# Performance work log

Hardware: AMD Instinct MI355X
Metric: run time of the kernel (lower is better)

The kernel has to match this reference:

```python
import jax, jax.numpy as jnp
import numpy as np

B, T, D, H, L = 8, 64, 128, 4, 4
G = B * T            # 512 frame-graphs
NPG = 200            # nodes per graph
N = G * NPG          # 102400 nodes
E = 8 * N            # 819200 edges
FIN, HID = 2, 64
DH = D // H
NCLS = 2


def setup_inputs():
    key = jax.random.key(0)
    ks = jax.random.split(key, 16)
    w = lambda k, s: (jax.random.normal(k, s) * 0.05).astype(jnp.float32)
    x = jax.random.normal(ks[0], (N, FIN), dtype=jnp.float32)
    g = jax.random.randint(ks[1], (E,), 0, G)
    src = (g * NPG + jax.random.randint(ks[2], (E,), 0, NPG)).astype(jnp.int32)
    dst = (g * NPG + jax.random.randint(ks[3], (E,), 0, NPG)).astype(jnp.int32)
    node_graph = (jnp.arange(N) // NPG).astype(jnp.int32)
    return dict(
        x=x, edge_src=src, edge_dst=dst, node_graph=node_graph,
        gW1=w(ks[4], (FIN, HID)), gb1=jnp.zeros((HID,), jnp.float32),
        ln1g=jnp.ones((HID,), jnp.float32), ln1b=jnp.zeros((HID,), jnp.float32),
        gW2=w(ks[5], (HID, HID)), gb2=jnp.zeros((HID,), jnp.float32),
        ln2g=jnp.ones((HID,), jnp.float32), ln2b=jnp.zeros((HID,), jnp.float32),
        gW3=w(ks[6], (HID, D)), gb3=jnp.zeros((D,), jnp.float32),
        tWqkv=w(ks[7], (L, 3 * D, D)), tbqkv=jnp.zeros((L, 3 * D), jnp.float32),
        tWo=w(ks[8], (L, D, D)), tbo=jnp.zeros((L, D), jnp.float32),
        tg1=jnp.ones((L, D), jnp.float32), tb1=jnp.zeros((L, D), jnp.float32),
        tg2=jnp.ones((L, D), jnp.float32), tb2=jnp.zeros((L, D), jnp.float32),
        tWf1=w(ks[9], (L, 4 * D, D)), tbf1=jnp.zeros((L, 4 * D), jnp.float32),
        tWf2=w(ks[10], (L, D, 4 * D)), tbf2=jnp.zeros((L, D), jnp.float32),
        hW1=w(ks[11], (D // 2, D)), hb1=jnp.zeros((D // 2,), jnp.float32),
        hW2=w(ks[12], (NCLS, D // 2)), hb2=jnp.zeros((NCLS,), jnp.float32),
    )


def _ln(x, g, b, eps=1e-5):
    m = jnp.mean(x, -1, keepdims=True)
    v = jnp.var(x, -1, keepdims=True)
    return (x - m) * jax.lax.rsqrt(v + eps) * g + b


def _forward(x, edge_src, edge_dst, node_graph, gW1, gb1, ln1g, ln1b, gW2, gb2,
             ln2g, ln2b, gW3, gb3, tWqkv, tbqkv, tWo, tbo, tg1, tb1, tg2, tb2,
             tWf1, tbf1, tWf2, tbf2, hW1, hb1, hW2, hb2):
    # --- GCN encoder (PyG GCNConv: sym-normalized A with self loops) ---
    loops = jnp.arange(N, dtype=jnp.int32)
    src = jnp.concatenate([edge_src, loops])
    dst = jnp.concatenate([edge_dst, loops])
    deg = jnp.zeros((N,), x.dtype).at[dst].add(1.0)
    dinv = jax.lax.rsqrt(deg)
    norm = (dinv[src] * dinv[dst])[:, None]

    def gcn(h, W, b):
        h = h @ W  # transform first (smaller message dim when FIN < HID)
        return jax.ops.segment_sum(h[src] * norm, dst, num_segments=N) + b

    h = _ln(jax.nn.relu(gcn(x, gW1, gb1)), ln1g, ln1b)
    h = _ln(jax.nn.relu(gcn(h, gW2, gb2)), ln2g, ln2b)
    h = gcn(h, gW3, gb3)  # (N, D)

    # per-graph mean readout (replaces the python loop in the original)
    cnt = jax.ops.segment_sum(jnp.ones((N,), h.dtype), node_graph, num_segments=G)
    emb = jax.ops.segment_sum(h, node_graph, num_segments=G) / cnt[:, None]
    seq = emb.reshape(B, T, D)

    # --- sinusoidal positional encoding ---
    pos = jnp.arange(T, dtype=jnp.float32)[:, None]
    div = jnp.exp(jnp.arange(0, D, 2, dtype=jnp.float32) * (-np.log(10000.0) / D))
    pe = jnp.zeros((T, D), jnp.float32)
    pe = pe.at[:, 0::2].set(jnp.sin(pos * div)).at[:, 1::2].set(jnp.cos(pos * div))
    seq = seq + pe

    # --- TransformerEncoder (post-norm, relu FFN, batch_first) ---
    scale = 1.0 / np.sqrt(DH)
    for l in range(L):
        qkv = seq @ tWqkv[l].T + tbqkv[l]
        q, k, v = jnp.split(qkv, 3, axis=-1)
        q = q.reshape(B, T, H, DH).transpose(0, 2, 1, 3)
        k = k.reshape(B, T, H, DH).transpose(0, 2, 1, 3)
        v = v.reshape(B, T, H, DH).transpose(0, 2, 1, 3)
        att = jax.nn.softmax(jnp.einsum('bhqd,bhkd->bhqk', q, k) * scale, axis=-1)
        a = jnp.einsum('bhqk,bhkd->bhqd', att, v).transpose(0, 2, 1, 3).reshape(B, T, D)
        seq = _ln(seq + a @ tWo[l].T + tbo[l], tg1[l], tb1[l])
        f = jax.nn.relu(seq @ tWf1[l].T + tbf1[l]) @ tWf2[l].T + tbf2[l]
        seq = _ln(seq + f, tg2[l], tb2[l])

    pooled = jnp.mean(seq, axis=1)  # mask=None path -> plain temporal mean
    return jax.nn.relu(pooled @ hW1.T + hb1) @ hW2.T + hb2  # (B, NCLS)


def reference(x, edge_src, edge_dst, node_graph, gW1, gb1, ln1g, ln1b, gW2, gb2,
              ln2g, ln2b, gW3, gb3, tWqkv, tbqkv, tWo, tbo, tg1, tb1, tg2, tb2,
              tWf1, tbf1, tWf2, tbf2, hW1, hb1, hW2, hb2):
    return _forward(x, edge_src, edge_dst, node_graph, gW1, gb1, ln1g, ln1b,
                    gW2, gb2, ln2g, ln2b, gW3, gb3, tWqkv, tbqkv, tWo, tbo,
                    tg1, tb1, tg2, tb2, tWf1, tbf1, tWf2, tbf2, hW1, hb1, hW2, hb2)
```

## Files before the change

### kernel.cpp

```cpp
#include <hip/hip_runtime.h>

#define NN   102400
#define EE   819200
#define GG   512
#define NPG  200
#define DD   128
#define TT   64
#define BB   8
#define LL   4
#define NB_A   320
#define ECH_A  2560
#define SCAP 2560
#define NSLOT 16
#define CHK  50

typedef unsigned int uint;

static __device__ __forceinline__ void wave_sum64_2(float& a, float& b) {
#pragma unroll
    for (int off = 32; off > 0; off >>= 1) {
        a += __shfl_xor(a, off, 64);
        b += __shfl_xor(b, off, 64);
    }
}


__global__ __launch_bounds__(256) void k_a1(const int* __restrict__ src,
                                            int* __restrict__ hist) {
    __shared__ int h[GG];
    int tid = threadIdx.x;
    h[tid] = 0; h[tid + 256] = 0;
    __syncthreads();
    int base = blockIdx.x * ECH_A;
#pragma unroll
    for (int it = 0; it < ECH_A / 256; ++it)
        atomicAdd(&h[src[base + it * 256 + tid] / NPG], 1);
    __syncthreads();
    hist[blockIdx.x * GG + tid] = h[tid];
    hist[blockIdx.x * GG + tid + 256] = h[tid + 256];
}

__global__ __launch_bounds__(64) void k_a2a(const int* __restrict__ hist,
                                            int* __restrict__ gcnt) {
    int g = blockIdx.x, lane = threadIdx.x;
    int s = 0;
#pragma unroll
    for (int i = 0; i < NB_A / 64; ++i) s += hist[(i * 64 + lane) * GG + g];
#pragma unroll
    for (int off = 32; off > 0; off >>= 1) s += __shfl_xor(s, off, 64);
    if (lane == 0) gcnt[g] = s;
}

__global__ __launch_bounds__(512) void k_a2b(const int* __restrict__ gcnt,
                                             int* __restrict__ goff) {
    __shared__ int sm[GG];
    int g = threadIdx.x;
    int c = gcnt[g];
    sm[g] = c;
    __syncthreads();
    for (int d = 1; d < GG; d <<= 1) {
        int v = (g >= d) ? sm[g - d] : 0;
        __syncthreads();
        sm[g] += v;
        __syncthreads();
    }
    goff[g] = sm[g] - c;
    if (g == GG - 1) goff[GG] = sm[g];
}

__global__ __launch_bounds__(512) void k_a2c(const int* __restrict__ hist,
                                             const int* __restrict__ goff,
                                             int* __restrict__ off2) {
    int g = blockIdx.x * 8 + (threadIdx.x >> 6);
    int lane = threadIdx.x & 63;
    int running = goff[g];
#pragma unroll
    for (int cchunk = 0; cchunk < NB_A / 64; ++cchunk) {
        int b = cchunk * 64 + lane;
        int v = hist[b * GG + g];
        int s = v;
#pragma unroll
        for (int off = 1; off < 64; off <<= 1) {
            int t_ = __shfl_up(s, off, 64);
            if (lane >= off) s += t_;
        }
        off2[b * GG + g] = running + s - v;
        running += __shfl(s, 63, 64);
    }
}

__global__ __launch_bounds__(256) void k_a3(const int* __restrict__ src,
                                            const int* __restrict__ dst,
                                            const int* __restrict__ off2,
                                            uint* __restrict__ gpack) {
    __shared__ int cur[GG];
    int tid = threadIdx.x;
    cur[tid] = off2[blockIdx.x * GG + tid];
    cur[tid + 256] = off2[blockIdx.x * GG + tid + 256];
    __syncthreads();
    int base = blockIdx.x * ECH_A;
#pragma unroll
    for (int it = 0; it < ECH_A / 256; ++it) {
        int e = base + it * 256 + tid;
        int s = src[e], d = dst[e];
        int g = s / NPG;
        int pos = atomicAdd(&cur[g], 1);
        gpack[pos] = ((uint)(s - g * NPG) << 8) | (uint)(d - g * NPG);
    }
}

__global__ __launch_bounds__(256) void k_bsort(
    const float* __restrict__ x, const int* __restrict__ goff,
    const uint* __restrict__ gpack, const float* __restrict__ W1,
    const float* __restrict__ gb1, const float* __restrict__ lng,
    const float* __restrict__ lnb, uint2* __restrict__ slots,
    uint2* __restrict__ ovf, int* __restrict__ ovfcnt,
    float* __restrict__ wgtv, float* __restrict__ hout) {
    int g = ((blockIdx.x & 7) << 6) | (blockIdx.x >> 3);
    __shared__ float2 xs[NPG];
    __shared__ float2 aggl[NPG];
    __shared__ int cnt2[NPG];
    __shared__ int lnoff[NPG + 1];
    __shared__ int cur[NPG];
    __shared__ float rsq[NPG];
    __shared__ float cwl[NPG];
    __shared__ uint srec[SCAP];
    __shared__ int sm[256];
    __shared__ uint2 ovfl[128];
    __shared__ int ovfcur;
    int tid = threadIdx.x;
    int base = goff[g], E = goff[g + 1] - base;
    const float2* x2 = (const float2*)x;
    if (tid < NPG) { xs[tid] = x2[g * NPG + tid]; cnt2[tid] = 0; cwl[tid] = 0.f; }
    if (tid == 0) ovfcur = 0;
    __syncthreads();
    for (int i = tid; i < E; i += 256) atomicAdd(&cnt2[gpack[base + i] & 255u], 1);
    __syncthreads();
    int c = (tid < NPG) ? cnt2[tid] : 0;
    sm[tid] = c;
    __syncthreads();
    for (int d = 1; d < 256; d <<= 1) {
        int v = (tid >= d) ? sm[tid - d] : 0;
        __syncthreads();
        sm[tid] += v;
        __syncthreads();
    }
    if (tid < NPG) {
        lnoff[tid] = sm[tid] - c;
        cur[tid] = sm[tid] - c;
        rsq[tid] = rsqrtf((float)(c + 1));
    }
    if (tid == 0) lnoff[NPG] = E;
    __syncthreads();
    for (int i = tid; i < E; i += 256) {
        uint r = gpack[base + i];
        int pos = atomicAdd(&cur[r & 255u], 1);
        srec[pos] = r;
    }
    __syncthreads();
    for (int i = tid; i < E; i += 256) {
        uint r = srec[i];
        atomicAdd(&cwl[r >> 8], rsq[r >> 8] * rsq[r & 255u]);
    }
    __syncthreads();
    {
        uint2* sbase = &slots[(size_t)g * NPG * NSLOT];
        for (int li = tid; li < NPG * NSLOT; li += 256) {
            int n = li >> 4, s = li & 15;
            int e0 = lnoff[n];
            int En = lnoff[n + 1] - e0;
            float rd = rsq[n];
            uint2 v;
            if (s == 0) {
                v = make_uint2((uint)(g * NPG + n), __float_as_uint(rd * rd));
            } else if (s - 1 < En) {
                uint r = srec[e0 + s - 1];
                int ls = (int)(r >> 8);
                v = make_uint2((uint)(g * NPG + ls), __float_as_uint(rsq[ls] * rd));
            } else {
                v = make_uint2((uint)(g * NPG + n), 0u);
            }
            sbase[li] = v;
        }
    }
    if (tid < NPG) {
        float rd = rsq[tid];
        float dv = rd * rd;
        float ax = xs[tid].x * dv, ay = xs[tid].y * dv;
        int e0 = lnoff[tid], e1 = lnoff[tid + 1];
        for (int e = e0; e < e1; ++e) {
            uint r = srec[e];
            int ls = (int)(r >> 8);
            float w = rsq[ls] * rd;
            ax += xs[ls].x * w;
            ay += xs[ls].y * w;
        }
        for (int e = e0 + NSLOT - 1; e < e1; ++e) {
            uint r = srec[e];
            int ls = (int)(r >> 8);
            int p = atomicAdd(&ovfcur, 1);
            if (p < 128)
                ovfl[p] = make_uint2(((uint)tid << 17) | (uint)(g * NPG + ls),
                                     __float_as_uint(rsq[ls] * rd));
        }
        aggl[tid] = make_float2(ax, ay);
        wgtv[g * NPG + tid] = cwl[tid] + dv;
    }
    __syncthreads();
    int nov = ovfcur < 128 ? ovfcur : 128;
    if (tid == 0) ovfcnt[g] = nov;
    if (tid < nov) ovf[g * 128 + tid] = ovfl[tid];
    int lane = tid & 63, wid = tid >> 6;
    float w0 = W1[lane], w1 = W1[64 + lane];
    float gbj = gb1[lane], lgj = lng[lane], lbj = lnb[lane];
    for (int i = wid; i < NPG; i += 4) {
        float2 a = aggl[i];
        float u = fmaxf(a.x * w0 + a.y * w1 + gbj, 0.f);
        float s2 = u, q2 = u * u;
        wave_sum64_2(s2, q2);
        float mean = s2 * (1.f / 64.f);
        float var = q2 * (1.f / 64.f) - mean * mean;
        hout[(size_t)(g * NPG + i) * 64 + lane] = (u - mean) * rsqrtf(var + 1e-5f) * lgj + lbj;
    }
}


__global__ __launch_bounds__(256) void k_agg_lin_pool(
    const float* __restrict__ t, const float* __restrict__ W,
    const float* __restrict__ gb, const float* __restrict__ lng,
    const float* __restrict__ lnb, const uint2* __restrict__ slots,
    const uint2* __restrict__ ovf, const int* __restrict__ ovfcnt,
    const float* __restrict__ wgtv, float* __restrict__ pooled) {
    int c = ((blockIdx.x & 7) << 8) | (blockIdx.x >> 3);
    int n0 = c * CHK;
    int g = c >> 2, lbase = (c & 3) * CHK;
    __shared__ float hs[CHK][64];
    __shared__ uint2 slt[CHK][NSLOT];
    __shared__ float wgt[CHK];
    __shared__ float red[4][64];
    int tid = threadIdx.x, lane = tid & 63, wid = tid >> 6;
    int grp = lane >> 4, fq = lane & 15;
    float wreg[64];
#pragma unroll
    for (int k = 0; k < 64; ++k) wreg[k] = W[k * 64 + lane];
    {
        const float4* s4 = (const float4*)&slots[(size_t)n0 * NSLOT];
        float4* d4 = (float4*)slt;
        for (int i = tid; i < CHK * NSLOT / 2; i += 256) d4[i] = s4[i];
    }
    if (tid < CHK) wgt[tid] = wgtv[n0 + tid];
    __syncthreads();
#pragma unroll 2
    for (int i = wid; i < CHK; i += 4) {
        float4 acc = make_float4(0.f, 0.f, 0.f, 0.f);
#pragma unroll
        for (int r = 0; r < 4; ++r) {
            uint2 s = slt[i][r * 4 + grp];
            float w = __uint_as_float(s.y);
            float4 tv = *(const float4*)&t[(size_t)s.x * 64 + fq * 4];
            acc.x += tv.x * w; acc.y += tv.y * w;
            acc.z += tv.z * w; acc.w += tv.w * w;
        }
        acc.x += __shfl_xor(acc.x, 16); acc.y += __shfl_xor(acc.y, 16);
        acc.z += __shfl_xor(acc.z, 16); acc.w += __shfl_xor(acc.w, 16);
        acc.x += __shfl_xor(acc.x, 32); acc.y += __shfl_xor(acc.y, 32);
        acc.z += __shfl_xor(acc.z, 32); acc.w += __shfl_xor(acc.w, 32);
        if (grp == 0) *(float4*)&hs[i][fq * 4] = acc;
    }
    __syncthreads();
    int nov = ovfcnt[g];
    if (nov && wid == 0) {
        for (int k = 0; k < nov; ++k) {
            uint2 r = ovf[g * 128 + k];
            int ld = r.x >> 17;
            if (ld >= lbase && ld < lbase + CHK)
                hs[ld - lbase][lane] +=
                    t[(size_t)(r.x & 0x1FFFFu) * 64 + lane] * __uint_as_float(r.y);
        }
    }
    __syncthreads();
    float gbj = gb[lane], lgj = lng[lane], lbj = lnb[lane];
    float psum = 0.f;
    for (int i = wid; i < CHK; i += 4) {
        const float4* hrow = (const float4*)&hs[i][0];
        float a0 = 0.f, a1 = 0.f;
#pragma unroll
        for (int k4 = 0; k4 < 16; k4 += 2) {
            float4 h0 = hrow[k4], h1 = hrow[k4 + 1];
            a0 += h0.x * wreg[4 * k4] + h0.y * wreg[4 * k4 + 1] +
                  h0.z * wreg[4 * k4 + 2] + h0.w * wreg[4 * k4 + 3];
            a1 += h1.x * wreg[4 * k4 + 4] + h1.y * wreg[4 * k4 + 5] +
                  h1.z * wreg[4 * k4 + 6] + h1.w * wreg[4 * k4 + 7];
        }
        float u = fmaxf(a0 + a1 + gbj, 0.f);
        float s = u, q = u * u;
        wave_sum64_2(s, q);
        float mean = s * (1.f / 64.f);
        float var = q * (1.f / 64.f) - mean * mean;
        float h = (u - mean) * rsqrtf(var + 1e-5f) * lgj + lbj;
        psum += h * wgt[i];
    }
    red[wid][lane] = psum;
    __syncthreads();
    if (tid < 64)
        atomicAdd(&pooled[g * 64 + tid],
                  red[0][tid] + red[1][tid] + red[2][tid] + red[3][tid]);
}

__global__ __launch_bounds__(128) void k_emb(
    const float* __restrict__ pooled, const float* __restrict__ W3,
    const float* __restrict__ b3, float* __restrict__ seq) {
    int g = blockIdx.x, d = threadIdx.x;
    __shared__ float ps[64];
    if (d < 64) ps[d] = pooled[g * 64 + d] * (1.f / NPG);
    __syncthreads();
    float a = b3[d];
#pragma unroll 8
    for (int k = 0; k < 64; ++k) a += ps[k] * W3[k * DD + d];
    float freq = expf((float)(d & ~1) * (-9.210340371976184f / 128.f));
    float ang = (float)(g & (TT - 1)) * freq;
    a += (d & 1) ? cosf(ang) : sinf(ang);
    seq[(size_t)g * DD + d] = a;
}


__global__ __launch_bounds__(128) void k_qkv(
    const float* __restrict__ seq, const float* __restrict__ Wqkv,
    const float* __restrict__ bqkv, float* __restrict__ qkvb) {
    int m = blockIdx.x, tid = threadIdx.x;
    __shared__ float row[128];
    row[tid] = seq[(size_t)m * DD + tid];
    __syncthreads();
    const float4* r4 = (const float4*)row;
    float acc0 = bqkv[tid], acc1 = bqkv[tid + 128], acc2 = bqkv[tid + 256];
    const float4* w0 = (const float4*)&Wqkv[(size_t)tid * DD];
    const float4* w1 = (const float4*)&Wqkv[(size_t)(tid + 128) * DD];
    const float4* w2 = (const float4*)&Wqkv[(size_t)(tid + 256) * DD];
#pragma unroll
    for (int k = 0; k < 32; ++k) {
        float4 a = r4[k];
        float4 x0 = w0[k], x1 = w1[k], x2 = w2[k];
        acc0 += a.x * x0.x + a.y * x0.y + a.z * x0.z + a.w * x0.w;
        acc1 += a.x * x1.x + a.y * x1.y + a.z * x1.z + a.w * x1.w;
        acc2 += a.x * x2.x + a.y * x2.y + a.z * x2.z + a.w * x2.w;
    }
    float* ob = qkvb + (size_t)m * 384;
    ob[tid] = acc0;
    ob[tid + 128] = acc1;
    ob[tid + 256] = acc2;
}

__global__ __launch_bounds__(256) void k_attn(const float* __restrict__ qkvb,
                                              float* __restrict__ abuf) {
    int bh = blockIdx.x >> 2, quad = blockIdx.x & 3;
    int b = bh >> 2, h = bh & 3;
    __shared__ float Ks[64][36], Vs[64][36];
    __shared__ float Ss[16][68];
    int tid = threadIdx.x;
    const float* base = qkvb + (size_t)(b * 64) * 384 + h * 32;
    for (int li = tid; li < 512; li += 256) {
        int r = li >> 3, cc = li & 7;
        *(float4*)&Ks[r][cc * 4] = *(const float4*)&base[(size_t)r * 384 + 128 + cc * 4];
        *(float4*)&Vs[r][cc * 4] = *(const float4*)&base[(size_t)r * 384 + 256 + cc * 4];
    }
    __syncthreads();
    int ql = tid >> 4, kl = tid & 15;
    int q = quad * 16 + ql;
    float qreg[32];
    {
        const float4* qp = (const float4*)&base[(size_t)q * 384];
#pragma unroll
        for (int i = 0; i < 8; ++i) {
            float4 v = qp[i];
            qreg[i * 4] = v.x; qreg[i * 4 + 1] = v.y;
            qreg[i * 4 + 2] = v.z; qreg[i * 4 + 3] = v.w;
        }
    }
    const float scale = 0.17677669529663687f;
    float p[4];
    float mx = -1e30f;
#pragma unroll
    for (int kk = 0; kk < 4; ++kk) {
        int k = kl * 4 + kk;
        float a = 0.f;
#pragma unroll
        for (int d = 0; d < 32; ++d) a += qreg[d] * Ks[k][d];
        p[kk] = a * scale;
        mx = fmaxf(mx, p[kk]);
    }
    mx = fmaxf(mx, __shfl_xor(mx, 1));
    mx = fmaxf(mx, __shfl_xor(mx, 2));
    mx = fmaxf(mx, __shfl_xor(mx, 4));
    mx = fmaxf(mx, __shfl_xor(mx, 8));
    float ssum = 0.f;
#pragma unroll
    for (int kk = 0; kk < 4; ++kk) {
        p[kk] = expf(p[kk] - mx);
        ssum += p[kk];
    }
    ssum += __shfl_xor(ssum, 1);
    ssum += __shfl_xor(ssum, 2);
    ssum += __shfl_xor(ssum, 4);
    ssum += __shfl_xor(ssum, 8);
    float inv = 1.f / ssum;
#pragma unroll
    for (int kk = 0; kk < 4; ++kk) Ss[ql][kl * 4 + kk] = p[kk] * inv;
    __syncthreads();
    int d0 = kl * 2;
    float o0 = 0.f, o1 = 0.f;
#pragma unroll 4
    for (int k = 0; k < 64; ++k) {
        float pw = Ss[ql][k];
        o0 += pw * Vs[k][d0];
        o1 += pw * Vs[k][d0 + 1];
    }
    float* op = abuf + (size_t)(b * 64 + q) * DD + h * 32 + d0;
    op[0] = o0;
    op[1] = o1;
}

__global__ __launch_bounds__(256) void k_post(
    const float* __restrict__ abuf, const float* __restrict__ Wo,
    const float* __restrict__ bo, const float* __restrict__ g1,
    const float* __restrict__ bl1, const float* __restrict__ Wf1,
    const float* __restrict__ bf1, const float* __restrict__ Wf2,
    const float* __restrict__ bf2, const float* __restrict__ g2,
    const float* __restrict__ bl2, float* __restrict__ seq) {
    int m0 = blockIdx.x * 2, tid = threadIdx.x;
    __shared__ float arow[2][128];
    __shared__ float srow[2][128];
    __shared__ float f1[2][512];
    __shared__ float pf[2][128];
    __shared__ float sred[4][2];
    __shared__ float sred2[2][4];
    int rr = tid >> 7, d0 = tid & 127;
    arow[rr][d0] = abuf[(size_t)(m0 + rr) * DD + d0];
    __syncthreads();
    {
        float acc = bo[d0];
        const float4* wr = (const float4*)&Wo[(size_t)d0 * DD];
        const float4* ar = (const float4*)arow[rr];
#pragma unroll
        for (int k = 0; k < 32; ++k) {
            float4 w = wr[k], a = ar[k];
            acc += a.x * w.x + a.y * w.y + a.z * w.z + a.w * w.w;
        }
        float u = seq[(size_t)(m0 + rr) * DD + d0] + acc;
        float s = u, q = u * u;
        wave_sum64_2(s, q);
        int wv = tid >> 6;
        if ((tid & 63) == 0) { sred[wv][0] = s; sred[wv][1] = q; }
        __syncthreads();
        int wp = rr * 2;
        s = sred[wp][0] + sred[wp + 1][0];
        q = sred[wp][1] + sred[wp + 1][1];
        float mean = s * (1.f / 128.f);
        float var = q * (1.f / 128.f) - mean * mean;
        float rstd = rsqrtf(var + 1e-5f);
        srow[rr][d0] = (u - mean) * rstd * g1[d0] + bl1[d0];
    }
    __syncthreads();
    const float4* s0 = (const float4*)srow[0];
    const float4* s1 = (const float4*)srow[1];
#pragma unroll
    for (int rep = 0; rep < 2; ++rep) {
        int o = tid + rep * 256;
        float bv = bf1[o];
        float a0 = bv, a1 = bv;
        const float4* wr = (const float4*)&Wf1[(size_t)o * DD];
#pragma unroll
        for (int k = 0; k < 32; ++k) {
            float4 w = wr[k];
            float4 x0 = s0[k], x1 = s1[k];
            a0 += x0.x * w.x + x0.y * w.y + x0.z * w.z + x0.w * w.w;
            a1 += x1.x * w.x + x1.y * w.y + x1.z * w.z + x1.w * w.w;
        }
        f1[0][o] = fmaxf(a0, 0.f);
        f1[1][o] = fmaxf(a1, 0.f);
    }
    __syncthreads();
    int d = tid & 127, half = tid >> 7;
    float b0 = half ? 0.f : bf2[d];
    float a0 = b0, a1 = b0;
    const float4* wr2 = (const float4*)&Wf2[(size_t)d * 512 + half * 256];
    const float4* f10 = (const float4*)&f1[0][half * 256];
    const float4* f11 = (const float4*)&f1[1][half * 256];
#pragma unroll
    for (int k = 0; k < 64; ++k) {
        float4 w = wr2[k];
        float4 x0 = f10[k], x1 = f11[k];
        a0 += x0.x * w.x + x0.y * w.y + x0.z * w.z + x0.w * w.w;
        a1 += x1.x * w.x + x1.y * w.y + x1.z * w.z + x1.w * w.w;
    }
    if (half) { pf[0][d] = a0; pf[1][d] = a1; }
    __syncthreads();
    if (half == 0) {
        float u0 = srow[0][d] + a0 + pf[0][d];
        float u1 = srow[1][d] + a1 + pf[1][d];
        float s0_ = u0, q0_ = u0 * u0, s1_ = u1, q1_ = u1 * u1;
        wave_sum64_2(s0_, q0_);
        wave_sum64_2(s1_, q1_);
        int w_ = d >> 6;
        if ((d & 63) == 0) {
            sred2[w_][0] = s0_; sred2[w_][1] = q0_;
            sred2[w_][2] = s1_; sred2[w_][3] = q1_;
        }
        __syncthreads();
        float S0 = sred2[0][0] + sred2[1][0], Q0 = sred2[0][1] + sred2[1][1];
        float S1 = sred2[0][2] + sred2[1][2], Q1 = sred2[0][3] + sred2[1][3];
        float mean0 = S0 * (1.f / 128.f);
        float var0 = Q0 * (1.f / 128.f) - mean0 * mean0;
        float rstd0 = rsqrtf(var0 + 1e-5f);
        float mean1 = S1 * (1.f / 128.f);
        float var1 = Q1 * (1.f / 128.f) - mean1 * mean1;
        float rstd1 = rsqrtf(var1 + 1e-5f);
        seq[(size_t)m0 * DD + d] = (u0 - mean0) * rstd0 * g2[d] + bl2[d];
        seq[(size_t)(m0 + 1) * DD + d] = (u1 - mean1) * rstd1 * g2[d] + bl2[d];
    } else {
        __syncthreads();
    }
}

__global__ __launch_bounds__(128) void k_head(
    const float* __restrict__ seq, const float* __restrict__ W1,
    const float* __restrict__ b1, const float* __restrict__ W2,
    const float* __restrict__ b2, float* __restrict__ out) {
    int b = blockIdx.x, t = threadIdx.x;
    __shared__ float pooled[DD];
    __shared__ float hid[64];
    float s = 0.f;
    for (int i = 0; i < TT; ++i) s += seq[(size_t)(b * TT + i) * DD + t];
    pooled[t] = s * (1.f / TT);
    __syncthreads();
    if (t < 64) {
        float a = b1[t];
        const float* wr = W1 + t * DD;
        for (int k = 0; k < DD; ++k) a += pooled[k] * wr[k];
        hid[t] = fmaxf(a, 0.f);
    }
    __syncthreads();
    if (t < 2) {
        float a = b2[t];
        const float* wr = W2 + t * 64;
        for (int k = 0; k < 64; ++k) a += hid[k] * wr[k];
        out[b * 2 + t] = a;
    }
}


extern "C" void kernel_launch(void* const* d_in, const int* in_sizes, int n_in,
                              void* d_out, int out_size, void* d_ws, size_t ws_size,
                              hipStream_t stream) {
    const float* x     = (const float*)d_in[0];
    const int*   esrc  = (const int*)d_in[1];
    const int*   edst  = (const int*)d_in[2];
    const float* gW1   = (const float*)d_in[4];
    const float* gb1   = (const float*)d_in[5];
    const float* ln1g  = (const float*)d_in[6];
    const float* ln1b  = (const float*)d_in[7];
    const float* gW2   = (const float*)d_in[8];
    const float* gb2   = (const float*)d_in[9];
    const float* ln2g  = (const float*)d_in[10];
    const float* ln2b  = (const float*)d_in[11];
    const float* gW3   = (const float*)d_in[12];
    const float* gb3   = (const float*)d_in[13];
    const float* tWqkv = (const float*)d_in[14];
    const float* tbqkv = (const float*)d_in[15];
    const float* tWo   = (const float*)d_in[16];
    const float* tbo   = (const float*)d_in[17];
    const float* tg1   = (const float*)d_in[18];
    const float* tb1   = (const float*)d_in[19];
    const float* tg2   = (const float*)d_in[20];
    const float* tb2   = (const float*)d_in[21];
    const float* tWf1  = (const float*)d_in[22];
    const float* tbf1  = (const float*)d_in[23];
    const float* tWf2  = (const float*)d_in[24];
    const float* tbf2  = (const float*)d_in[25];
    const float* hW1   = (const float*)d_in[26];
    const float* hb1   = (const float*)d_in[27];
    const float* hW2   = (const float*)d_in[28];
    const float* hb2   = (const float*)d_in[29];
    float* out = (float*)d_out;

    int*   hist   = (int*)d_ws;
    int*   off2   = hist + NB_A * GG;
    int*   gcnt   = off2 + NB_A * GG;
    int*   goff   = gcnt + GG;
    uint*  gpack  = (uint*)(goff + 516);
    uint2* slots  = (uint2*)(gpack + EE);
    uint2* ovf    = slots + (size_t)NN * NSLOT;
    int*   ovfcnt = (int*)(ovf + GG * 128);
    float* wgtv   = (float*)(ovfcnt + GG);
    float* pooled = wgtv + NN;
    float* bufA = pooled + GG * 64;
    float* seq  = bufA + (size_t)NN * 64;
    float* qkvb = seq + GG * DD;
    float* abuf = qkvb + GG * 384;

    hipMemsetAsync(pooled, 0, GG * 64 * sizeof(float), stream);
    k_a1<<<NB_A, 256, 0, stream>>>(esrc, hist);
    k_a2a<<<GG, 64, 0, stream>>>(hist, gcnt);
    k_a2b<<<1, 512, 0, stream>>>(gcnt, goff);
    k_a2c<<<64, 512, 0, stream>>>(hist, goff, off2);
    k_a3<<<NB_A, 256, 0, stream>>>(esrc, edst, off2, gpack);
    k_bsort<<<GG, 256, 0, stream>>>(x, goff, gpack, gW1, gb1, ln1g, ln1b,
                                    slots, ovf, ovfcnt, wgtv, bufA);

    k_agg_lin_pool<<<NN / CHK, 256, 0, stream>>>(bufA, gW2, gb2, ln2g, ln2b,
                                                 slots, ovf, ovfcnt, wgtv, pooled);
    k_emb<<<GG, DD, 0, stream>>>(pooled, gW3, gb3, seq);

    for (int l = 0; l < LL; l++) {
        k_qkv<<<GG, 128, 0, stream>>>(
            seq, tWqkv + (size_t)l * 384 * 128, tbqkv + l * 384, qkvb);
        k_attn<<<BB * 4 * 4, 256, 0, stream>>>(qkvb, abuf);
        k_post<<<GG / 2, 256, 0, stream>>>(
            abuf, tWo + (size_t)l * 128 * 128, tbo + l * 128,
            tg1 + l * 128, tb1 + l * 128,
            tWf1 + (size_t)l * 512 * 128, tbf1 + l * 512,
            tWf2 + (size_t)l * 128 * 512, tbf2 + l * 128,
            tg2 + l * 128, tb2 + l * 128, seq);
    }

    k_head<<<BB, DD, 0, stream>>>(seq, hW1, hb1, hW2, hb2, out);
}
```

Before: 331.3 us.

## Fuse aggregation, overflow handling and linear layer in registers via shuffles

Removes the shared-memory hs staging buffer and the two barriers between aggregation, overflow correction and the 64x64 linear layer. Each wave now applies overflow edges to its own row from an LDS copy of the overflow list, then broadcasts the row's aggregated features with __shfl to do the matvec against weights held in registers. This cuts LDS traffic and synchronisation and adds launch_bounds(256,2) for occupancy. In exchange it costs many shuffles per row and a per-row scan of the overflow list.

```diff
diff --git a/kernel.cpp b/kernel.cpp
--- a/kernel.cpp
+++ b/kernel.cpp
@@ -225,7 +225,25 @@
 }
 
 
-__global__ __launch_bounds__(256) void k_agg_lin_pool(
+#define LDW8(B) \
+    const float wA##B##0 = Wl[(B * 8 + 0) * 64]; \
+    const float wA##B##1 = Wl[(B * 8 + 1) * 64]; \
+    const float wA##B##2 = Wl[(B * 8 + 2) * 64]; \
+    const float wA##B##3 = Wl[(B * 8 + 3) * 64]; \
+    const float wA##B##4 = Wl[(B * 8 + 4) * 64]; \
+    const float wA##B##5 = Wl[(B * 8 + 5) * 64]; \
+    const float wA##B##6 = Wl[(B * 8 + 6) * 64]; \
+    const float wA##B##7 = Wl[(B * 8 + 7) * 64];
+
+#define STEP2(KQ, WA, WB, WC, WD, WE, WF, WG2, WH) { \
+    float z0 = __shfl(acc.x, (KQ)), z1 = __shfl(acc.y, (KQ)); \
+    float z2 = __shfl(acc.z, (KQ)), z3 = __shfl(acc.w, (KQ)); \
+    float y0 = __shfl(acc.x, (KQ) + 1), y1 = __shfl(acc.y, (KQ) + 1); \
+    float y2 = __shfl(acc.z, (KQ) + 1), y3 = __shfl(acc.w, (KQ) + 1); \
+    o0 += z0 * WA; o1 += z1 * WB; o2 += z2 * WC; o3 += z3 * WD; \
+    o0 += y0 * WE; o1 += y1 * WF; o2 += y2 * WG2; o3 += y3 * WH; }
+
+__global__ __launch_bounds__(256, 2) void k_agg_lin_pool(
     const float* __restrict__ t, const float* __restrict__ W,
     const float* __restrict__ gb, const float* __restrict__ lng,
     const float* __restrict__ lnb, const uint2* __restrict__ slots,
@@ -234,23 +252,25 @@
     int c = ((blockIdx.x & 7) << 8) | (blockIdx.x >> 3);
     int n0 = c * CHK;
     int g = c >> 2, lbase = (c & 3) * CHK;
-    __shared__ float hs[CHK][64];
     __shared__ uint2 slt[CHK][NSLOT];
     __shared__ float wgt[CHK];
+    __shared__ uint2 ovfs[128];
     __shared__ float red[4][64];
     int tid = threadIdx.x, lane = tid & 63, wid = tid >> 6;
     int grp = lane >> 4, fq = lane & 15;
-    float wreg[64];
-#pragma unroll
-    for (int k = 0; k < 64; ++k) wreg[k] = W[k * 64 + lane];
+    const float* Wl = W + lane;
+    LDW8(0) LDW8(1) LDW8(2) LDW8(3) LDW8(4) LDW8(5) LDW8(6) LDW8(7)
     {
         const float4* s4 = (const float4*)&slots[(size_t)n0 * NSLOT];
         float4* d4 = (float4*)slt;
         for (int i = tid; i < CHK * NSLOT / 2; i += 256) d4[i] = s4[i];
     }
     if (tid < CHK) wgt[tid] = wgtv[n0 + tid];
-    __syncthreads();
-#pragma unroll 2
+    int nov = ovfcnt[g];
+    if (tid < nov) ovfs[tid] = ovf[g * 128 + tid];
+    __syncthreads();
+    float gbj = gb[lane], lgj = lng[lane], lbj = lnb[lane];
+    float psum = 0.f;
     for (int i = wid; i < CHK; i += 4) {
         float4 acc = make_float4(0.f, 0.f, 0.f, 0.f);
 #pragma unroll
@@ -265,34 +285,25 @@
         acc.z += __shfl_xor(acc.z, 16); acc.w += __shfl_xor(acc.w, 16);
         acc.x += __shfl_xor(acc.x, 32); acc.y += __shfl_xor(acc.y, 32);
         acc.z += __shfl_xor(acc.z, 32); acc.w += __shfl_xor(acc.w, 32);
-        if (grp == 0) *(float4*)&hs[i][fq * 4] = acc;
-    }
-    __syncthreads();
-    int nov = ovfcnt[g];
-    if (nov && wid == 0) {
         for (int k = 0; k < nov; ++k) {
-            uint2 r = ovf[g * 128 + k];
-            int ld = r.x >> 17;
-            if (ld >= lbase && ld < lbase + CHK)
-                hs[ld - lbase][lane] +=
-                    t[(size_t)(r.x & 0x1FFFFu) * 64 + lane] * __uint_as_float(r.y);
-        }
-    }
-    __syncthreads();
-    float gbj = gb[lane], lgj = lng[lane], lbj = lnb[lane];
-    float psum = 0.f;
-    for (int i = wid; i < CHK; i += 4) {
-        const float4* hrow = (const float4*)&hs[i][0];
-        float a0 = 0.f, a1 = 0.f;
-#pragma unroll
-        for (int k4 = 0; k4 < 16; k4 += 2) {
-            float4 h0 = hrow[k4], h1 = hrow[k4 + 1];
-            a0 += h0.x * wreg[4 * k4] + h0.y * wreg[4 * k4 + 1] +
-                  h0.z * wreg[4 * k4 + 2] + h0.w * wreg[4 * k4 + 3];
-            a1 += h1.x * wreg[4 * k4 + 4] + h1.y * wreg[4 * k4 + 5] +
-                  h1.z * wreg[4 * k4 + 6] + h1.w * wreg[4 * k4 + 7];
-        }
-        float u = fmaxf(a0 + a1 + gbj, 0.f);
+            uint2 r = ovfs[k];
+            if ((int)(r.x >> 17) == lbase + i) {
+                float w = __uint_as_float(r.y);
+                float4 tv = *(const float4*)&t[(size_t)(r.x & 0x1FFFFu) * 64 + fq * 4];
+                acc.x += tv.x * w; acc.y += tv.y * w;
+                acc.z += tv.z * w; acc.w += tv.w * w;
+            }
+        }
+        float o0 = 0.f, o1 = 0.f, o2 = 0.f, o3 = 0.f;
+        STEP2(0,  wA00, wA01, wA02, wA03, wA04, wA05, wA06, wA07)
+        STEP2(2,  wA10, wA11, wA12, wA13, wA14, wA15, wA16, wA17)
+        STEP2(4,  wA20, wA21, wA22, wA23, wA24, wA25, wA26, wA27)
+        STEP2(6,  wA30, wA31, wA32, wA33, wA34, wA35, wA36, wA37)
+        STEP2(8,  wA40, wA41, wA42, wA43, wA44, wA45, wA46, wA47)
+        STEP2(10, wA50, wA51, wA52, wA53, wA54, wA55, wA56, wA57)
+        STEP2(12, wA60, wA61, wA62, wA63, wA64, wA65, wA66, wA67)
+        STEP2(14, wA70, wA71, wA72, wA73, wA74, wA75, wA76, wA77)
+        float u = fmaxf(o0 + o1 + o2 + o3 + gbj, 0.f);
         float s = u, q = u * u;
         wave_sum64_2(s, q);
         float mean = s * (1.f / 64.f);
```

Measured after the change: 386.3 us. 1.17x slower.
